# Kernel optimization log

Hardware: AMD Instinct MI355X
Metric: run time of the kernel (lower is better)

The kernel has to match this reference:

```python
import jax, jax.numpy as jnp
import numpy as np

B, LAT, D = 64, 256, 64           # batch, latent dim, voxel grid side (== output image side)
ALPHA_ADJ = float(np.log2(D) + 2)  # alpha_adjust = log2(output_img_shape[0]) + 2


def _rotmat(a):
    """3x3 rotation matrix from Euler angles (x,y,z), R = Rz @ Ry @ Rx."""
    cx, sx = jnp.cos(a[0]), jnp.sin(a[0])
    cy, sy = jnp.cos(a[1]), jnp.sin(a[1])
    cz, sz = jnp.cos(a[2]), jnp.sin(a[2])
    Rx = jnp.array([[1, 0, 0], [0, 0, 0], [0, 0, 0]], jnp.float32).at[1, 1].set(cx).at[1, 2].set(-sx).at[2, 1].set(sx).at[2, 2].set(cx)
    Ry = jnp.array([[0, 0, 0], [0, 1, 0], [0, 0, 0]], jnp.float32).at[0, 0].set(cy).at[0, 2].set(sy).at[2, 0].set(-sy).at[2, 2].set(cy)
    Rz = jnp.array([[0, 0, 0], [0, 0, 0], [0, 0, 1]], jnp.float32).at[0, 0].set(cz).at[0, 1].set(-sz).at[1, 0].set(sz).at[1, 1].set(cz)
    return Rz @ Ry @ Rx


def _apply_transform(vol, R):
    """Rotate a [D,D,D] volume about its centre via trilinear sampling, zero padding."""
    d = vol.shape[0]
    c = (d - 1) / 2.0
    idx = jnp.arange(d, dtype=jnp.float32)
    gi, gj, gk = jnp.meshgrid(idx, idx, idx, indexing='ij')
    dst = jnp.stack([gi, gj, gk], axis=-1) - c        # [D,D,D,3]
    src = dst @ R.T + c                                # source coords
    x, y, z = src[..., 0], src[..., 1], src[..., 2]
    x0 = jnp.floor(x); y0 = jnp.floor(y); z0 = jnp.floor(z)
    fx, fy, fz = x - x0, y - y0, z - z0

    def gather(ix, iy, iz):
        valid = (ix >= 0) & (ix < d) & (iy >= 0) & (iy < d) & (iz >= 0) & (iz < d)
        ixc = jnp.clip(ix, 0, d - 1).astype(jnp.int32)
        iyc = jnp.clip(iy, 0, d - 1).astype(jnp.int32)
        izc = jnp.clip(iz, 0, d - 1).astype(jnp.int32)
        return jnp.where(valid, vol[ixc, iyc, izc], 0.0)

    c000 = gather(x0, y0, z0);     c001 = gather(x0, y0, z0 + 1)
    c010 = gather(x0, y0 + 1, z0); c011 = gather(x0, y0 + 1, z0 + 1)
    c100 = gather(x0 + 1, y0, z0); c101 = gather(x0 + 1, y0, z0 + 1)
    c110 = gather(x0 + 1, y0 + 1, z0); c111 = gather(x0 + 1, y0 + 1, z0 + 1)
    c00 = c000 * (1 - fz) + c001 * fz
    c01 = c010 * (1 - fz) + c011 * fz
    c10 = c100 * (1 - fz) + c101 * fz
    c11 = c110 * (1 - fz) + c111 * fz
    c0 = c00 * (1 - fy) + c01 * fy
    c1 = c10 * (1 - fy) + c11 * fy
    return c0 * (1 - fx) + c1 * fx


def setup_inputs() -> dict:
    key = jax.random.key(0)
    k1, k2, k3 = jax.random.split(key, 3)
    encoded = jax.random.normal(k1, (B, LAT), dtype=jnp.float32)
    W = jax.random.normal(k2, (LAT, D * D * D), dtype=jnp.float32) * 0.02
    b = jnp.zeros((D * D * D,), jnp.float32)
    angles = jax.random.uniform(k3, (B, 3), jnp.float32, -np.pi, np.pi)
    return {"encoded": encoded, "W": W, "b": b, "angles": angles}


def reference(encoded, W, b, angles):
    # voxel_generator: linear -> sigmoid -> [B, D, D, D], then alpha sharpening
    voxels = jax.nn.sigmoid(encoded @ W + b).reshape(B, D, D, D)
    voxels = voxels ** ALPHA_ADJ
    R = jax.vmap(_rotmat)(angles)                       # [B,3,3]
    views = jax.vmap(_apply_transform)(voxels, R)       # [B,D,D,D]
    # alpha compositing back-to-front along last (depth) axis
    alphas = jnp.moveaxis(views, -1, 0)[:, :, None]     # [Dz, B, 1, H, W]
    def step(img, a):
        return img * (1 - a) + a, None
    images, _ = jax.lax.scan(step, jnp.zeros((B, 1, D, D), jnp.float32), alphas, reverse=True)
    return 2 * images - 1
```

## Files before the change

### kernel.cpp

```cpp
#include <hip/hip_runtime.h>
#include <hip/hip_bf16.h>
#include <hip/hip_fp16.h>
#include <math.h>

#define BATCH 64
#define LAT   256
#define DVOX  64
#define VOX   (DVOX*DVOX*DVOX)

typedef __attribute__((ext_vector_type(8))) short short8;
typedef __attribute__((ext_vector_type(4))) float f32x4;
typedef unsigned uint32x4 __attribute__((ext_vector_type(4), aligned(4)));

__global__ void prep_kernel(const float* __restrict__ enc,
                            const float* __restrict__ angles,
                            unsigned short* __restrict__ encB,
                            float* __restrict__ Rmat) {
    int tid = threadIdx.x;
    for (int idx = tid; idx < BATCH * LAT; idx += blockDim.x) {
        __hip_bfloat16 h = __float2bfloat16(enc[idx]);
        encB[idx] = *reinterpret_cast<unsigned short*>(&h);
    }
    if (tid < BATCH) {
        float ax = angles[tid*3+0], ay = angles[tid*3+1], az = angles[tid*3+2];
        float cx = cosf(ax), sx = sinf(ax);
        float cy = cosf(ay), sy = sinf(ay);
        float cz = cosf(az), sz = sinf(az);
        float* R = Rmat + tid * 9;
        R[0] = cz*cy;  R[1] = cz*sy*sx - sz*cx;  R[2] = cz*sy*cx + sz*sx;
        R[3] = sz*cy;  R[4] = sz*sy*sx + cz*cx;  R[5] = sz*sy*cx - cz*sx;
        R[6] = -sy;    R[7] = cy*sx;             R[8] = cy*cx;
    }
}

__global__ __launch_bounds__(256, 2) void gemm_mfma_kernel(
        const unsigned short* __restrict__ encB,
        const float* __restrict__ W,
        const float* __restrict__ bias,
        __half* __restrict__ vox) {
    int wave = threadIdx.x >> 6;
    int lane = threadIdx.x & 63;
    int l15 = lane & 15, l4 = lane >> 4;
    int n4 = blockIdx.x * 256 + wave * 64 + 4 * l15;

    f32x4 acc[4][4];
#pragma unroll
    for (int t = 0; t < 4; ++t)
#pragma unroll
        for (int mt = 0; mt < 4; ++mt) acc[t][mt] = (f32x4){0.f, 0.f, 0.f, 0.f};

    const unsigned short* ap = encB + l15 * LAT + l4 * 8;
    const float* wp = W + (size_t)(l4 * 8) * VOX + n4;

    float4 wA[8], wB[8];
#pragma unroll
    for (int j = 0; j < 8; ++j)
        wA[j] = *(const float4*)(wp + (size_t)j * VOX);

    auto consume = [&](const float4* w, int kb) {
        short8 a[4];
#pragma unroll
        for (int mt = 0; mt < 4; ++mt)
            a[mt] = *(const short8*)(ap + mt * 16 * LAT + kb);
        short8 bf[4];
#pragma unroll
        for (int t = 0; t < 4; ++t) {
            unsigned bw[4];
#pragma unroll
            for (int dw = 0; dw < 4; ++dw) {
                unsigned u0 = __float_as_uint(((const float*)&w[2 * dw])[t])     + 0x8000u;
                unsigned u1 = __float_as_uint(((const float*)&w[2 * dw + 1])[t]) + 0x8000u;
                bw[dw] = __builtin_amdgcn_perm(u1, u0, 0x07060302u);
            }
            bf[t] = *reinterpret_cast<short8*>(bw);
        }
#pragma unroll
        for (int t = 0; t < 4; ++t)
#pragma unroll
            for (int mt = 0; mt < 4; ++mt)
                acc[t][mt] = __builtin_amdgcn_mfma_f32_16x16x32_bf16(a[mt], bf[t], acc[t][mt], 0, 0, 0);
    };

#pragma unroll
    for (int kb2 = 0; kb2 < LAT; kb2 += 64) {
        {
            const float* q = wp + (size_t)(kb2 + 32) * VOX;
#pragma unroll
            for (int j = 0; j < 8; ++j) wB[j] = *(const float4*)(q + (size_t)j * VOX);
        }
        consume(wA, kb2);
        if (kb2 + 64 < LAT) {
            const float* q = wp + (size_t)(kb2 + 64) * VOX;
#pragma unroll
            for (int j = 0; j < 8; ++j) wA[j] = *(const float4*)(q + (size_t)j * VOX);
        }
        consume(wB, kb2 + 32);
    }

    float4 bv = *(const float4*)(bias + n4);
#pragma unroll
    for (int mt = 0; mt < 4; ++mt) {
#pragma unroll
        for (int r = 0; r < 4; ++r) {
            int b = mt * 16 + l4 * 4 + r;
            float s[4];
#pragma unroll
            for (int t = 0; t < 4; ++t) {
                float x = acc[t][mt][r] + ((const float*)&bv)[t];
                float v = 1.f / (1.f + __expf(-x));
                v = v * v; v = v * v; v = v * v;
                s[t] = v;
            }
            __half2 h01 = __floats2half2_rn(s[0], s[1]);
            __half2 h23 = __floats2half2_rn(s[2], s[3]);
            uint2 pk;
            pk.x = *reinterpret_cast<unsigned*>(&h01);
            pk.y = *reinterpret_cast<unsigned*>(&h23);
            *reinterpret_cast<uint2*>(vox + (size_t)b * VOX + n4) = pk;
        }
    }
}

__device__ __forceinline__ float zlerp(unsigned e, float fz) {
    __half2 h = *reinterpret_cast<__half2*>(&e);
    float2 f = __half22float2(h);
    return f.x + (f.y - f.x) * fz;
}

__global__ __launch_bounds__(256) void render_lds_kernel(
        const __half* __restrict__ vox,
        const float* __restrict__ Rmat,
        float* __restrict__ out) {
    __shared__ unsigned sV[16 * 16 * 17];
    __shared__ float sT[4][64], sE[4][64];

    int bid  = blockIdx.x;
    int b    = bid & 63;
    int tile = bid >> 6;
    int t    = threadIdx.x;
    int pix  = t & 63, seg = t >> 6;
    int i0 = (tile >> 3) * 8, j0 = (tile & 7) * 8;
    int i = i0 + (pix >> 3);
    int j = j0 + (pix & 7);

    const float* Rb = Rmat + b * 9;
    float R0 = Rb[0], R1 = Rb[1], R2 = Rb[2];
    float R3 = Rb[3], R4 = Rb[4], R5 = Rb[5];
    float R6 = Rb[6], R7 = Rb[7], R8 = Rb[8];

    const float c = (DVOX - 1) * 0.5f;
    float di = (float)i - c, dj = (float)j - c;
    float xb = fmaf(R0, di, fmaf(R1, dj, c));
    float yb = fmaf(R3, di, fmaf(R4, dj, c));
    float zb = fmaf(R6, di, fmaf(R7, dj, c));

    float dic = (float)i0 + 3.5f - c;
    float djc = (float)j0 + 3.5f - c;
    float hwx = 3.5f * (fabsf(R0) + fabsf(R1) + fabsf(R2)) + 1e-3f;
    float hwy = 3.5f * (fabsf(R3) + fabsf(R4) + fabsf(R5)) + 1e-3f;
    float hwz = 3.5f * (fabsf(R6) + fabsf(R7) + fabsf(R8)) + 1e-3f;

    const unsigned short* V = (const unsigned short*)vox + (size_t)b * VOX;

    int rx = t >> 4, ry = t & 15;
    unsigned d[9];
    int xlo_n, ylo_n, zlo_n, s_n;

    auto bbox = [&](int ch) {
        float dkc = (float)(ch * 8) + 3.5f - c;
        float xc = fmaf(R0, dic, fmaf(R1, djc, fmaf(R2, dkc, c)));
        float yc = fmaf(R3, dic, fmaf(R4, djc, fmaf(R5, dkc, c)));
        float zc = fmaf(R6, dic, fmaf(R7, djc, fmaf(R8, dkc, c)));
        xlo_n = (int)floorf(xc - hwx);
        ylo_n = (int)floorf(yc - hwy);
        zlo_n = (int)floorf(zc - hwz);
        s_n   = zlo_n & ~1;
    };
    auto issue = [&]() {
        int gxc = min(max(xlo_n + rx, 0), DVOX - 1);
        int gyc = min(max(ylo_n + ry, 0), DVOX - 1);
        const unsigned* p = (const unsigned*)(V + ((gxc << 12) + (gyc << 6) + s_n));
        uint32x4 q0 = *(const uint32x4*)p;
        uint32x4 q1 = *(const uint32x4*)(p + 4);
        unsigned q2 = p[8];
        d[0] = q0[0]; d[1] = q0[1]; d[2] = q0[2]; d[3] = q0[3];
        d[4] = q1[0]; d[5] = q1[1]; d[6] = q1[2]; d[7] = q1[3];
        d[8] = q2;
    };

    bbox(7); issue();
    int xlo = xlo_n, ylo = ylo_n, zlo = zlo_n, s = s_n;

    float img = 0.f;
#pragma unroll 1
    for (int ch = 7; ch >= 0; --ch) {
        bool zint = (zlo >= 0) && (zlo + 17 <= DVOX);

        {
            bool rv = ((unsigned)(xlo + rx) < (unsigned)DVOX) &
                      ((unsigned)(ylo + ry) < (unsigned)DVOX);
            unsigned tt[9];
#pragma unroll
            for (int k = 0; k < 9; ++k) tt[k] = d[k];
            if (!zint) {
#pragma unroll
                for (int k = 0; k < 9; ++k) {
                    int h0 = s + 2 * k;
                    unsigned m = (((unsigned)h0 < (unsigned)DVOX) ? 0x0000FFFFu : 0u)
                               | (((unsigned)(h0 + 1) < (unsigned)DVOX) ? 0xFFFF0000u : 0u);
                    tt[k] &= m;
                }
            }
            unsigned rvm = rv ? 0xFFFFFFFFu : 0u;
#pragma unroll
            for (int k = 0; k < 9; ++k) tt[k] &= rvm;

            unsigned A[8];
#pragma unroll
            for (int m = 0; m < 8; ++m)
                A[m] = (tt[m] >> 16) | (tt[m + 1] << 16);

            unsigned* wrow = sV + t * 17;
            if (zlo & 1) {
#pragma unroll
                for (int m = 0; m < 8; ++m) {
                    wrow[2 * m]     = A[m];
                    wrow[2 * m + 1] = tt[m + 1];
                }
            } else {
#pragma unroll
                for (int m = 0; m < 8; ++m) {
                    wrow[2 * m]     = tt[m];
                    wrow[2 * m + 1] = A[m];
                }
            }
        }
        __syncthreads();

        if (ch > 0) { bbox(ch - 1); issue(); }

        float T = 1.f, E = 0.f;
        int k0 = ch * 8;
#pragma unroll
        for (int q = 1; q >= 0; --q) {
            int kk = 2 * seg + q;
            float dk = (float)(k0 + kk) - c;
            float x = fmaf(R2, dk, xb);
            float y = fmaf(R5, dk, yb);
            float z = fmaf(R8, dk, zb);

            float xf = floorf(x), yf = floorf(y), zf = floorf(z);
            float fx = x - xf, fy = y - yf, fz = z - zf;
            int xi = (int)xf - xlo;
            int yi = (int)yf - ylo;
            int zi = (int)zf - zlo;
            const unsigned* e = sV + (xi * 272 + yi * 17 + zi);

            float c00 = zlerp(e[0],   fz);
            float c01 = zlerp(e[17],  fz);
            float c10 = zlerp(e[272], fz);
            float c11 = zlerp(e[289], fz);
            float c0 = c00 + (c01 - c00) * fy;
            float c1 = c10 + (c11 - c10) * fy;
            float a  = c0  + (c1  - c0 ) * fx;

            E = E * (1.f - a) + a;
            T *= (1.f - a);
        }
        sT[seg][pix] = T;
        sE[seg][pix] = E;
        __syncthreads();

        if (seg == 0) {
            float im = img;
#pragma unroll
            for (int ss = 3; ss >= 0; --ss)
                im = fmaf(sT[ss][pix], im, sE[ss][pix]);
            img = im;
        }

        xlo = xlo_n; ylo = ylo_n; zlo = zlo_n; s = s_n;
    }

    if (seg == 0)
        out[b * (DVOX * DVOX) + i * DVOX + j] = 2.f * img - 1.f;
}

extern "C" void kernel_launch(void* const* d_in, const int* in_sizes, int n_in,
                              void* d_out, int out_size, void* d_ws, size_t ws_size,
                              hipStream_t stream) {
    const float* enc    = (const float*)d_in[0];
    const float* W      = (const float*)d_in[1];
    const float* bias   = (const float*)d_in[2];
    const float* angles = (const float*)d_in[3];
    float* out = (float*)d_out;

    char* ws = (char*)d_ws;
    unsigned short* encB = (unsigned short*)ws;
    float* Rmat          = (float*)(ws + 32768);
    __half* vox          = (__half*)(ws + 65536);

    prep_kernel<<<1, 256, 0, stream>>>(enc, angles, encB, Rmat);
    gemm_mfma_kernel<<<VOX / 256, 256, 0, stream>>>(encB, W, bias, vox);
    render_lds_kernel<<<BATCH * 64, 256, 0, stream>>>(vox, Rmat, out);
}
```

Before: 142.2 us.

## Stage W tiles through LDS with async global_load_lds double buffering

After: 142.2 us. No clear change (-0.0%).

```diff
diff --git a/kernel.cpp b/kernel.cpp
--- a/kernel.cpp
+++ b/kernel.cpp
@@ -33,15 +33,32 @@
     }
 }
 
+#define KT    32
+#define LROW  260
+#define LBUF  8352
+
+__device__ __forceinline__ void gload_lds16(const float* g, unsigned* l) {
+    __builtin_amdgcn_global_load_lds(
+        (__attribute__((address_space(1))) void*)(g),
+        (__attribute__((address_space(3))) void*)(l),
+        16, 0, 0);
+}
+
 __global__ __launch_bounds__(256, 2) void gemm_mfma_kernel(
         const unsigned short* __restrict__ encB,
         const float* __restrict__ W,
         const float* __restrict__ bias,
         __half* __restrict__ vox) {
+    __shared__ unsigned lds[2 * LBUF];
+
     int wave = threadIdx.x >> 6;
     int lane = threadIdx.x & 63;
     int l15 = lane & 15, l4 = lane >> 4;
-    int n4 = blockIdx.x * 256 + wave * 64 + 4 * l15;
+    int n0 = blockIdx.x * 256;
+    int n4 = n0 + wave * 64 + 4 * l15;
+
+    const unsigned short* ap = encB + l15 * LAT + l4 * 8;
+    const float* gb = W + n0 + lane * 4;
 
     f32x4 acc[4][4];
 #pragma unroll
@@ -49,27 +66,44 @@
 #pragma unroll
         for (int mt = 0; mt < 4; ++mt) acc[t][mt] = (f32x4){0.f, 0.f, 0.f, 0.f};
 
-    const unsigned short* ap = encB + l15 * LAT + l4 * 8;
-    const float* wp = W + (size_t)(l4 * 8) * VOX + n4;
-
-    float4 wA[8], wB[8];
-#pragma unroll
-    for (int j = 0; j < 8; ++j)
-        wA[j] = *(const float4*)(wp + (size_t)j * VOX);
-
-    auto consume = [&](const float4* w, int kb) {
+    auto stage = [&](int buf, int kb) {
+        unsigned* lb = lds + buf * LBUF;
+#pragma unroll
+        for (int i = 0; i < 8; ++i) {
+            int row = i * 4 + wave;
+            gload_lds16(gb + (size_t)(kb + row) * VOX,
+                        lb + row * LROW + ((row >> 3) & 3) * 8);
+        }
+    };
+
+    stage(0, 0);
+
+#pragma unroll
+    for (int kt = 0; kt < 8; ++kt) {
+        __syncthreads();
+        if (kt < 7) stage((kt + 1) & 1, (kt + 1) * KT);
+
         short8 a[4];
 #pragma unroll
         for (int mt = 0; mt < 4; ++mt)
-            a[mt] = *(const short8*)(ap + mt * 16 * LAT + kb);
+            a[mt] = *(const short8*)(ap + mt * 16 * LAT + kt * KT);
+
+        const unsigned* lb = lds + (kt & 1) * LBUF
+                           + (l4 * 8) * LROW + l4 * 8
+                           + wave * 64 + 4 * l15;
+        uint4 dj[8];
+#pragma unroll
+        for (int j = 0; j < 8; ++j)
+            dj[j] = *(const uint4*)(lb + j * LROW);
+
         short8 bf[4];
 #pragma unroll
         for (int t = 0; t < 4; ++t) {
             unsigned bw[4];
 #pragma unroll
             for (int dw = 0; dw < 4; ++dw) {
-                unsigned u0 = __float_as_uint(((const float*)&w[2 * dw])[t])     + 0x8000u;
-                unsigned u1 = __float_as_uint(((const float*)&w[2 * dw + 1])[t]) + 0x8000u;
+                unsigned u0 = ((const unsigned*)&dj[2 * dw])[t]     + 0x8000u;
+                unsigned u1 = ((const unsigned*)&dj[2 * dw + 1])[t] + 0x8000u;
                 bw[dw] = __builtin_amdgcn_perm(u1, u0, 0x07060302u);
             }
             bf[t] = *reinterpret_cast<short8*>(bw);
@@ -79,22 +113,6 @@
 #pragma unroll
             for (int mt = 0; mt < 4; ++mt)
                 acc[t][mt] = __builtin_amdgcn_mfma_f32_16x16x32_bf16(a[mt], bf[t], acc[t][mt], 0, 0, 0);
-    };
-
-#pragma unroll
-    for (int kb2 = 0; kb2 < LAT; kb2 += 64) {
-        {
-            const float* q = wp + (size_t)(kb2 + 32) * VOX;
-#pragma unroll
-            for (int j = 0; j < 8; ++j) wB[j] = *(const float4*)(q + (size_t)j * VOX);
-        }
-        consume(wA, kb2);
-        if (kb2 + 64 < LAT) {
-            const float* q = wp + (size_t)(kb2 + 64) * VOX;
-#pragma unroll
-            for (int j = 0; j < 8; ++j) wA[j] = *(const float4*)(q + (size_t)j * VOX);
-        }
-        consume(wB, kb2 + 32);
     }
 
     float4 bv = *(const float4*)(bias + n4);
```
